# Performance work log

Measured on AMD Instinct MI355X. Metric: run time of the kernel, lower is better.

The kernel has to match this reference:

```python
import jax, jax.numpy as jnp
import numpy as np

B = 8192          # batch
CIN = 256         # in_channels
COUT = 64         # out_channels
K = 3             # kernel_size
NK = 4            # num_kernels
HIDDEN = int(CIN * 0.25)   # attention hidden = int(in_channels*ratio) = 64
TEMP = 34.0       # attention temperature
KAN_IN = 64 * 4   # base*4 = flattened conv output (COUT*2*2)
GRID_SIZE, SPLINE_ORDER = 5, 3
GMIN, GMAX = -1.0, 1.0
NUM_BASES = GRID_SIZE + SPLINE_ORDER  # 8


def setup_inputs() -> dict:
    key = jax.random.key(0)
    ks = jax.random.split(key, 8)
    s = 0.05
    return {
        "x": jax.random.normal(ks[0], (B, CIN, 4, 4), jnp.float32),
        # dynamic-conv kernel bank [num_kernels, out, in, k, k]
        "weight": jax.random.normal(ks[1], (NK, COUT, CIN, K, K), jnp.float32) * s,
        "bias": jnp.zeros((NK, COUT), jnp.float32),
        # Attention2D: GAP -> fc1 (1x1 conv == linear) -> ReLU -> fc2 -> softmax(/T)
        "fc1_w": jax.random.normal(ks[2], (HIDDEN, CIN), jnp.float32) * s,
        "fc1_b": jnp.zeros((HIDDEN,), jnp.float32),
        "fc2_w": jax.random.normal(ks[3], (NK, HIDDEN), jnp.float32) * s,
        "fc2_b": jnp.zeros((NK,), jnp.float32),
        # KANLinear params (efficient-KAN style)
        "kan_base_w": jax.random.normal(ks[4], (COUT, KAN_IN), jnp.float32) * s,
        "kan_spline_w": jax.random.normal(ks[5], (COUT, KAN_IN, NUM_BASES), jnp.float32) * s,
        "kan_spline_scaler": jnp.ones((COUT, KAN_IN), jnp.float32),
    }


def _bspline_bases(x):
    """Cox-de Boor B-spline bases; x [B, F] -> [B, F, GRID_SIZE+SPLINE_ORDER]."""
    h = (GMAX - GMIN) / GRID_SIZE
    # extended grid, shared across features: length grid_size + 2*order + 1 = 12
    grid = jnp.arange(-SPLINE_ORDER, GRID_SIZE + SPLINE_ORDER + 1, dtype=x.dtype) * h + GMIN
    xe = x[..., None]  # [B, F, 1]
    bases = ((xe >= grid[:-1]) & (xe < grid[1:])).astype(x.dtype)  # order 0
    for k in range(1, SPLINE_ORDER + 1):
        left = (xe - grid[: -(k + 1)]) / (grid[k:-1] - grid[: -(k + 1)]) * bases[..., :-1]
        right = (grid[k + 1:] - xe) / (grid[k + 1:] - grid[1:-k]) * bases[..., 1:]
        bases = left + right
    return bases  # [B, F, 8]


def reference(x, weight, bias, fc1_w, fc1_b, fc2_w, fc2_b,
              kan_base_w, kan_spline_w, kan_spline_scaler):
    b = x.shape[0]
    # --- Attention2D: softmax over kernel bank ---
    pooled = x.mean(axis=(2, 3))                                  # [B, CIN]
    hid = jax.nn.relu(pooled @ fc1_w.T + fc1_b)                   # [B, HIDDEN]
    attn = jax.nn.softmax((hid @ fc2_w.T + fc2_b) / TEMP, axis=-1)  # [B, NK]
    # --- per-sample dynamic conv, fused form ---
    # sum_k a[b,k] * conv(x, W_k) == conv with per-sample aggregated weight
    w_all = weight.reshape(NK * COUT, CIN, K, K)
    y = jax.lax.conv_general_dilated(
        x, w_all, window_strides=(1, 1), padding="VALID",
        dimension_numbers=("NCHW", "OIHW", "NCHW"))                # [B, NK*COUT, 2, 2]
    y = y.reshape(b, NK, COUT, y.shape[-2], y.shape[-1])
    conv_out = jnp.einsum("bk,bkohw->bohw", attn, y)
    conv_out = conv_out + (attn @ bias)[:, :, None, None]          # aggregated bias
    # --- KANLinear on flattened conv output ---
    feat = conv_out.reshape(b, -1)                                 # [B, 256]
    base_out = jax.nn.silu(feat) @ kan_base_w.T                    # [B, COUT]
    bases = _bspline_bases(feat)                                   # [B, 256, 8]
    spline_out = jnp.einsum("big,oig->bo", bases,
                            kan_spline_w * kan_spline_scaler[..., None])
    return base_out + spline_out                                   # [B, COUT]
```

## Files before the change

kernel.cpp:

```cpp
#include <hip/hip_runtime.h>

#define BT   8192
#define MS   16
#define XBUF (MS * 656)

typedef _Float16 half8  __attribute__((ext_vector_type(8)));
typedef _Float16 half4v __attribute__((ext_vector_type(4)));
typedef float    floatx4  __attribute__((ext_vector_type(4)));
typedef float    floatx16 __attribute__((ext_vector_type(16)));

__global__ __launch_bounds__(256) void prep_kernel(
    const float* __restrict__ weight, const float* __restrict__ base_w,
    const float* __restrict__ spline_w, const float* __restrict__ scaler,
    const float* __restrict__ fc1_w,
    _Float16* __restrict__ W3, _Float16* __restrict__ Wk3,
    _Float16* __restrict__ Wf3)
{
    const int bb = blockIdx.x;
    const int tid = threadIdx.x;
    if (bb < 256) {
        const int n = bb;
        const int c = tid;
        const float* src = weight + ((size_t)n * 256 + c) * 9;
        const int cc = c >> 5, ci = c & 31;
        #pragma unroll
        for (int ij = 0; ij < 9; ++ij) {
            W3[((size_t)(cc * 9 + ij) * 256 + n) * 32 + ci] = (_Float16)src[ij];
        }
    } else if (bb < 328) {
        const int st = bb - 256;
        #pragma unroll
        for (int u = 0; u < 8; ++u) {
            const int idx = u * 256 + tid;
            const int n = idx >> 5, kk = idx & 31;
            const int k = st * 32 + kk;
            float v;
            if (k < 256) {
                v = base_w[n * 256 + k];
            } else {
                const int r = k - 256;
                const int i = r >> 3, g = r & 7;
                v = spline_w[((size_t)n * 256 + i) * 8 + g] * scaler[n * 256 + i];
            }
            Wk3[(size_t)st * 2048 + idx] = (_Float16)v;
        }
    } else {
        const int st2 = bb - 328;
        #pragma unroll
        for (int u = 0; u < 8; ++u) {
            const int idx = u * 256 + tid;
            const int n = idx >> 5, kk = idx & 31;
            Wf3[(size_t)st2 * 2048 + idx] = (_Float16)fc1_w[n * 256 + st2 * 32 + kk];
        }
    }
}

__device__ __forceinline__ void bases8c(float xv, _Float16* dst) {
    const float t = (xv + 2.2f) * 2.5f;
    const float ft = floorf(t);
    const int idx = (int)ft;
    const float u = t - ft, v = 1.f - u;
    const float u2 = u * u, v2 = v * v;
    const float c3 = u2 * u * (1.f / 6.f);
    const float c2 = (1.f / 6.f) + 0.5f * (u + u2 - u2 * u);
    const float c1 = (1.f / 6.f) + 0.5f * (v + v2 - v2 * v);
    const float c0 = v2 * v * (1.f / 6.f);
    half8 hb;
    #pragma unroll
    for (int tt = 0; tt < 8; ++tt) {
        const int d = idx - tt;
        float b = 0.f;
        b = (d == 0) ? c3 : b;
        b = (d == 1) ? c2 : b;
        b = (d == 2) ? c1 : b;
        b = (d == 3) ? c0 : b;
        hb[tt] = (_Float16)b;
    }
    *(half8*)dst = hb;
}

__global__ __launch_bounds__(512, 4) void fused_kernel(
    const float* __restrict__ x, const _Float16* __restrict__ W3,
    const _Float16* __restrict__ Wk3, const _Float16* __restrict__ Wf3,
    const float* __restrict__ bias, const float* __restrict__ fc1_b,
    const float* __restrict__ fc2_w, const float* __restrict__ fc2_b,
    float* __restrict__ out)
{
    __shared__ __align__(16) char smem[MS * 2312 * 2];
    __shared__ float hid_lds[MS * 68];
    __shared__ float attn_s[MS][4];

    _Float16* Xs  = (_Float16*)smem;
    _Float16* Pl  = (_Float16*)(smem + 2 * XBUF * 2);
    _Float16* Act = (_Float16*)smem;

    const int tid = threadIdx.x;
    const int wv = tid >> 6, lane = tid & 63;
    const int nl = lane & 15, q = lane >> 4;
    const int cg = wv & 3, rh = wv >> 2;
    const int b0i = blockIdx.x * MS;

    const int posr = nl & 3;
    const int aLane = (nl >> 2) * 656 + ((posr >> 1) * 4 + (posr & 1)) * 40 + q * 8;
    const int lbW0 = (((rh * 2 + 0) * 4 + cg) * 16 + nl) * 32 + q * 8;
    const int lbW1 = (((rh * 2 + 1) * 4 + cg) * 16 + nl) * 32 + q * 8;

    const int s_ = tid >> 5, cch = tid & 31;
    const float* xg = x + ((size_t)(b0i + s_) * 256 + cch) * 16;

    floatx4 acc[4][2];
    #pragma unroll
    for (int rt = 0; rt < 4; ++rt) {
        acc[rt][0] = floatx4{0.f, 0.f, 0.f, 0.f};
        acc[rt][1] = floatx4{0.f, 0.f, 0.f, 0.f};
    }

    half8 bA0 = *(const half8*)(W3 + lbW0);
    half8 bB0 = *(const half8*)(W3 + lbW1);
    half8 bA1 = *(const half8*)(W3 + 8192 + lbW0);
    half8 bB1 = *(const half8*)(W3 + 8192 + lbW1);

    floatx16 r = *(const floatx16*)xg;
    {
        _Float16* xd = &Xs[s_ * 656 + cch];
        #pragma unroll
        for (int p = 0; p < 16; ++p) xd[p * 40] = (_Float16)r[p];
        float sm = 0.f;
        #pragma unroll
        for (int p = 0; p < 16; ++p) sm += r[p];
        Pl[s_ * 264 + cch] = (_Float16)(sm * (1.0f / 16.0f));
    }
    r = *(const floatx16*)(xg + 512);
    __syncthreads();

    #pragma unroll 1
    for (int cc = 0; cc < 8; ++cc) {
        const int cur = cc & 1;
        if (cc < 7) {
            _Float16* xd = &Xs[(cur ^ 1) * XBUF + s_ * 656 + cch];
            #pragma unroll
            for (int p = 0; p < 16; ++p) xd[p * 40] = (_Float16)r[p];
            float sm = 0.f;
            #pragma unroll
            for (int p = 0; p < 16; ++p) sm += r[p];
            Pl[s_ * 264 + (cc + 1) * 32 + cch] = (_Float16)(sm * (1.0f / 16.0f));
        }
        if (cc < 6) r = *(const floatx16*)(xg + (cc + 2) * 512);

        const _Float16* wst = W3 + (size_t)cc * 9 * 8192;
        const _Float16* xb = &Xs[cur * XBUF + aLane];

        const int p0tab[9] = {0, 1, 2, 4, 5, 6, 8, 9, 10};

        half8 aC0 = *(const half8*)&xb[0 * 2624];
        half8 aC1 = *(const half8*)&xb[1 * 2624];
        half8 aC2 = *(const half8*)&xb[2 * 2624];
        half8 aC3 = *(const half8*)&xb[3 * 2624];

        #pragma unroll
        for (int ij = 0; ij < 9; ++ij) {
            half8 bA2, bB2;
            {
                const _Float16* wnx = (cc * 9 + ij + 2 < 72)
                                    ? (wst + (size_t)(ij + 2) * 8192)
                                    : W3;
                bA2 = *(const half8*)(wnx + lbW0);
                bB2 = *(const half8*)(wnx + lbW1);
            }
            half8 aN0, aN1, aN2, aN3;
            if (ij < 8) {
                const int pn = p0tab[ij + 1] * 40;
                aN0 = *(const half8*)&xb[0 * 2624 + pn];
                aN1 = *(const half8*)&xb[1 * 2624 + pn];
                aN2 = *(const half8*)&xb[2 * 2624 + pn];
                aN3 = *(const half8*)&xb[3 * 2624 + pn];
            }
            acc[0][0] = __builtin_amdgcn_mfma_f32_16x16x32_f16(aC0, bA0, acc[0][0], 0, 0, 0);
            acc[0][1] = __builtin_amdgcn_mfma_f32_16x16x32_f16(aC0, bB0, acc[0][1], 0, 0, 0);
            acc[1][0] = __builtin_amdgcn_mfma_f32_16x16x32_f16(aC1, bA0, acc[1][0], 0, 0, 0);
            acc[1][1] = __builtin_amdgcn_mfma_f32_16x16x32_f16(aC1, bB0, acc[1][1], 0, 0, 0);
            acc[2][0] = __builtin_amdgcn_mfma_f32_16x16x32_f16(aC2, bA0, acc[2][0], 0, 0, 0);
            acc[2][1] = __builtin_amdgcn_mfma_f32_16x16x32_f16(aC2, bB0, acc[2][1], 0, 0, 0);
            acc[3][0] = __builtin_amdgcn_mfma_f32_16x16x32_f16(aC3, bA0, acc[3][0], 0, 0, 0);
            acc[3][1] = __builtin_amdgcn_mfma_f32_16x16x32_f16(aC3, bB0, acc[3][1], 0, 0, 0);
            bA0 = bA1; bB0 = bB1; bA1 = bA2; bB1 = bB2;
            if (ij < 8) { aC0 = aN0; aC1 = aN1; aC2 = aN2; aC3 = aN3; }
        }
        __syncthreads();
    }

    if (rh == 0) {
        floatx4 a1 = floatx4{0.f, 0.f, 0.f, 0.f};
        const _Float16* wfb = Wf3 + ((cg * 16 + nl) * 32 + q * 8);
        const _Float16* pb = &Pl[nl * 264 + q * 8];
        #pragma unroll
        for (int st = 0; st < 8; ++st) {
            const half8 aF = *(const half8*)(pb + st * 32);
            const half8 bF = *(const half8*)(wfb + st * 2048);
            a1 = __builtin_amdgcn_mfma_f32_16x16x32_f16(aF, bF, a1, 0, 0, 0);
        }
        const int h = cg * 16 + nl;
        const float fb = fc1_b[h];
        #pragma unroll
        for (int reg = 0; reg < 4; ++reg)
            hid_lds[(q * 4 + reg) * 68 + h] = fmaxf(a1[reg] + fb, 0.f);
    }
    __syncthreads();

    if (wv == 0) {
        const int s = lane >> 2, kb = lane & 3;
        float l = fc2_b[kb];
        #pragma unroll 8
        for (int h = 0; h < 64; ++h) l += hid_lds[s * 68 + h] * fc2_w[kb * 64 + h];
        float m = fmaxf(l, __shfl_xor(l, 1));
        m = fmaxf(m, __shfl_xor(m, 2));
        const float e = __expf((l - m) * (1.0f / 34.0f));
        float sm = e + __shfl_xor(e, 1);
        sm += __shfl_xor(sm, 2);
        attn_s[s][kb] = e / sm;
    }
    __syncthreads();

    const int o = cg * 16 + nl;
    if (rh == 1) {
        #pragma unroll
        for (int rt = 0; rt < 4; ++rt) {
            const int s = rt * 4 + q;
            const float a2w = attn_s[s][2], a3w = attn_s[s][3];
            #pragma unroll
            for (int e = 0; e < 4; ++e) {
                float* slot = (float*)&Act[s * 2312 + 256 + (o * 4 + e) * 8];
                slot[0] = a2w * acc[rt][0][e] + a3w * acc[rt][1][e];
            }
        }
    }
    __syncthreads();

    if (rh == 0) {
        const float bb0 = bias[o], bb1 = bias[64 + o], bb2 = bias[128 + o], bb3 = bias[192 + o];
        #pragma unroll
        for (int rt = 0; rt < 4; ++rt) {
            const int s = rt * 4 + q;
            const float a0 = attn_s[s][0], a1 = attn_s[s][1],
                        a2 = attn_s[s][2], a3 = attn_s[s][3];
            const float badd = a0 * bb0 + a1 * bb1 + a2 * bb2 + a3 * bb3;
            float f[4];
            #pragma unroll
            for (int e = 0; e < 4; ++e) {
                const float part = ((float*)&Act[s * 2312 + 256 + (o * 4 + e) * 8])[0];
                f[e] = a0 * acc[rt][0][e] + a1 * acc[rt][1][e] + part + badd;
            }
            half4v sv;
            #pragma unroll
            for (int e = 0; e < 4; ++e) {
                const float ex = __expf(-f[e]);
                sv[e] = (_Float16)(f[e] * __builtin_amdgcn_rcpf(1.f + ex));
            }
            *(half4v*)&Act[s * 2312 + o * 4] = sv;
            #pragma unroll
            for (int e = 0; e < 4; ++e)
                bases8c(f[e], &Act[s * 2312 + 256 + (o * 4 + e) * 8]);
        }
    }
    __syncthreads();

    {
        floatx4 a2 = floatx4{0.f, 0.f, 0.f, 0.f};
        const _Float16* wkb = Wk3 + ((size_t)(cg * 16 + nl) * 32 + q * 8);
        const _Float16* ab = &Act[nl * 2312 + q * 8];
        const int st0 = rh * 36;
        half8 kb0 = *(const half8*)(wkb + (size_t)st0 * 2048);
        half8 kb1 = *(const half8*)(wkb + (size_t)(st0 + 1) * 2048);
        #pragma unroll 4
        for (int i = 0; i < 36; ++i) {
            half8 kb2;
            if (i < 34) kb2 = *(const half8*)(wkb + (size_t)(st0 + i + 2) * 2048);
            const half8 aF = *(const half8*)(ab + (st0 + i) * 32);
            a2 = __builtin_amdgcn_mfma_f32_16x16x32_f16(aF, kb0, a2, 0, 0, 0);
            kb0 = kb1; kb1 = kb2;
        }
        if (rh == 1) *(floatx4*)&hid_lds[cg * 256 + lane * 4] = a2;
        __syncthreads();
        if (rh == 0) {
            const floatx4 p = *(const floatx4*)&hid_lds[cg * 256 + lane * 4];
            a2 = a2 + p;
            #pragma unroll
            for (int reg = 0; reg < 4; ++reg)
                out[(size_t)(b0i + q * 4 + reg) * 64 + cg * 16 + nl] = a2[reg];
        }
    }
}

extern "C" void kernel_launch(void* const* d_in, const int* in_sizes, int n_in,
                              void* d_out, int out_size, void* d_ws, size_t ws_size,
                              hipStream_t stream) {
    const float* x          = (const float*)d_in[0];
    const float* weight     = (const float*)d_in[1];
    const float* bias       = (const float*)d_in[2];
    const float* fc1_w      = (const float*)d_in[3];
    const float* fc1_b      = (const float*)d_in[4];
    const float* fc2_w      = (const float*)d_in[5];
    const float* fc2_b      = (const float*)d_in[6];
    const float* kan_base_w = (const float*)d_in[7];
    const float* kan_spline = (const float*)d_in[8];
    const float* kan_scaler = (const float*)d_in[9];
    float* out = (float*)d_out;

    _Float16* W3  = (_Float16*)d_ws;
    _Float16* Wk3 = W3 + (size_t)72 * 8192;
    _Float16* Wf3 = Wk3 + (size_t)72 * 2048;

    prep_kernel<<<336, 256, 0, stream>>>(weight, kan_base_w, kan_spline,
                                         kan_scaler, fc1_w, W3, Wk3, Wf3);
    fused_kernel<<<BT / MS, 512, 0, stream>>>(x, W3, Wk3, Wf3, bias, fc1_b,
                                              fc2_w, fc2_b, out);
}
```

Baseline: 246.6 us.

## Vectorize x staging with shuffle pooling and split epilogue across all waves

The x staging now uses floatx4 loads and half4 LDS stores, and the pooled means are reduced with cross-lane shuffles instead of per-thread sums over 16 scalars. The epilogue changes too: both row-halves write raw accumulator partials to LDS, and all 8 waves then compute the attention-weighted combine, SiLU and B-spline bases, each thread handling 8 features of one sample. This drops one barrier and the idle half of the waves in the epilogue. The A-operand prefetch in the MFMA loop is removed in favour of direct loads each iteration, which may expose LDS latency.

```diff
diff --git a/kernel.cpp b/kernel.cpp
--- a/kernel.cpp
+++ b/kernel.cpp
@@ -6,8 +6,8 @@
 
 typedef _Float16 half8  __attribute__((ext_vector_type(8)));
 typedef _Float16 half4v __attribute__((ext_vector_type(4)));
+typedef float    floatx2  __attribute__((ext_vector_type(2)));
 typedef float    floatx4  __attribute__((ext_vector_type(4)));
-typedef float    floatx16 __attribute__((ext_vector_type(16)));
 
 __global__ __launch_bounds__(256) void prep_kernel(
     const float* __restrict__ weight, const float* __restrict__ base_w,
@@ -105,8 +105,9 @@
     const int lbW0 = (((rh * 2 + 0) * 4 + cg) * 16 + nl) * 32 + q * 8;
     const int lbW1 = (((rh * 2 + 1) * 4 + cg) * 16 + nl) * 32 + q * 8;
 
-    const int s_ = tid >> 5, cch = tid & 31;
-    const float* xg = x + ((size_t)(b0i + s_) * 256 + cch) * 16;
+    const int s_ = tid >> 5, w32 = tid & 31;
+    const int qd = w32 & 7, pq = w32 >> 3;
+    const float* xg = x + ((size_t)(b0i + s_) * 256 + qd * 4) * 16 + pq * 4;
 
     floatx4 acc[4][2];
     #pragma unroll
@@ -120,71 +121,82 @@
     half8 bA1 = *(const half8*)(W3 + 8192 + lbW0);
     half8 bB1 = *(const half8*)(W3 + 8192 + lbW1);
 
-    floatx16 r = *(const floatx16*)xg;
-    {
-        _Float16* xd = &Xs[s_ * 656 + cch];
-        #pragma unroll
-        for (int p = 0; p < 16; ++p) xd[p * 40] = (_Float16)r[p];
-        float sm = 0.f;
-        #pragma unroll
-        for (int p = 0; p < 16; ++p) sm += r[p];
-        Pl[s_ * 264 + cch] = (_Float16)(sm * (1.0f / 16.0f));
-    }
-    r = *(const floatx16*)(xg + 512);
+    floatx4 r0, r1, r2, r3;
+    #define STAGE_POOL(bf, ch)                                             \
+    {                                                                      \
+        _Float16* xd = &Xs[(bf) * XBUF + s_ * 656 + qd * 4];               \
+        _Pragma("unroll")                                                  \
+        for (int pl = 0; pl < 4; ++pl) {                                   \
+            half4v w;                                                      \
+            w[0] = (_Float16)r0[pl]; w[1] = (_Float16)r1[pl];              \
+            w[2] = (_Float16)r2[pl]; w[3] = (_Float16)r3[pl];              \
+            *(half4v*)&xd[(pq * 4 + pl) * 40] = w;                         \
+        }                                                                  \
+        float p0s = r0[0] + r0[1] + r0[2] + r0[3];                         \
+        float p1s = r1[0] + r1[1] + r1[2] + r1[3];                         \
+        float p2s = r2[0] + r2[1] + r2[2] + r2[3];                         \
+        float p3s = r3[0] + r3[1] + r3[2] + r3[3];                         \
+        p0s += __shfl_xor(p0s, 8);  p1s += __shfl_xor(p1s, 8);             \
+        p2s += __shfl_xor(p2s, 8);  p3s += __shfl_xor(p3s, 8);             \
+        p0s += __shfl_xor(p0s, 16); p1s += __shfl_xor(p1s, 16);            \
+        p2s += __shfl_xor(p2s, 16); p3s += __shfl_xor(p3s, 16);            \
+        if (pq == 0) {                                                     \
+            half4v pw;                                                     \
+            pw[0] = (_Float16)(p0s * 0.0625f);                             \
+            pw[1] = (_Float16)(p1s * 0.0625f);                             \
+            pw[2] = (_Float16)(p2s * 0.0625f);                             \
+            pw[3] = (_Float16)(p3s * 0.0625f);                             \
+            *(half4v*)&Pl[s_ * 264 + (ch) * 32 + qd * 4] = pw;             \
+        }                                                                  \
+    }
+
+    r0 = *(const floatx4*)(xg);
+    r1 = *(const floatx4*)(xg + 16);
+    r2 = *(const floatx4*)(xg + 32);
+    r3 = *(const floatx4*)(xg + 48);
+    STAGE_POOL(0, 0)
+    r0 = *(const floatx4*)(xg + 512);
+    r1 = *(const floatx4*)(xg + 512 + 16);
+    r2 = *(const floatx4*)(xg + 512 + 32);
+    r3 = *(const floatx4*)(xg + 512 + 48);
     __syncthreads();
 
     #pragma unroll 1
     for (int cc = 0; cc < 8; ++cc) {
         const int cur = cc & 1;
-        if (cc < 7) {
-            _Float16* xd = &Xs[(cur ^ 1) * XBUF + s_ * 656 + cch];
-            #pragma unroll
-            for (int p = 0; p < 16; ++p) xd[p * 40] = (_Float16)r[p];
-            float sm = 0.f;
-            #pragma unroll
-            for (int p = 0; p < 16; ++p) sm += r[p];
-            Pl[s_ * 264 + (cc + 1) * 32 + cch] = (_Float16)(sm * (1.0f / 16.0f));
-        }
-        if (cc < 6) r = *(const floatx16*)(xg + (cc + 2) * 512);
+        if (cc < 7) STAGE_POOL(cur ^ 1, cc + 1)
+        if (cc < 6) {
+            const float* xn = xg + (cc + 2) * 512;
+            r0 = *(const floatx4*)(xn);
+            r1 = *(const floatx4*)(xn + 16);
+            r2 = *(const floatx4*)(xn + 32);
+            r3 = *(const floatx4*)(xn + 48);
+        }
 
         const _Float16* wst = W3 + (size_t)cc * 9 * 8192;
         const _Float16* xb = &Xs[cur * XBUF + aLane];
 
         const int p0tab[9] = {0, 1, 2, 4, 5, 6, 8, 9, 10};
 
-        half8 aC0 = *(const half8*)&xb[0 * 2624];
-        half8 aC1 = *(const half8*)&xb[1 * 2624];
-        half8 aC2 = *(const half8*)&xb[2 * 2624];
-        half8 aC3 = *(const half8*)&xb[3 * 2624];
-
         #pragma unroll
         for (int ij = 0; ij < 9; ++ij) {
-            half8 bA2, bB2;
-            {
-                const _Float16* wnx = (cc * 9 + ij + 2 < 72)
-                                    ? (wst + (size_t)(ij + 2) * 8192)
-                                    : W3;
-                bA2 = *(const half8*)(wnx + lbW0);
-                bB2 = *(const half8*)(wnx + lbW1);
+            const _Float16* wnx = (cc * 9 + ij + 2 < 72)
+                                ? (wst + (size_t)(ij + 2) * 8192)
+                                : W3;
+            half8 bA2 = *(const half8*)(wnx + lbW0);
+            half8 bB2 = *(const half8*)(wnx + lbW1);
+
+            const int p0 = p0tab[ij];
+            half8 aF[4];
+            #pragma unroll
+            for (int rt = 0; rt < 4; ++rt)
+                aF[rt] = *(const half8*)&xb[rt * 2624 + p0 * 40];
+            #pragma unroll
+            for (int rt = 0; rt < 4; ++rt) {
+                acc[rt][0] = __builtin_amdgcn_mfma_f32_16x16x32_f16(aF[rt], bA0, acc[rt][0], 0, 0, 0);
+                acc[rt][1] = __builtin_amdgcn_mfma_f32_16x16x32_f16(aF[rt], bB0, acc[rt][1], 0, 0, 0);
             }
-            half8 aN0, aN1, aN2, aN3;
-            if (ij < 8) {
-                const int pn = p0tab[ij + 1] * 40;
-                aN0 = *(const half8*)&xb[0 * 2624 + pn];
-                aN1 = *(const half8*)&xb[1 * 2624 + pn];
-                aN2 = *(const half8*)&xb[2 * 2624 + pn];
-                aN3 = *(const half8*)&xb[3 * 2624 + pn];
-            }
-            acc[0][0] = __builtin_amdgcn_mfma_f32_16x16x32_f16(aC0, bA0, acc[0][0], 0, 0, 0);
-            acc[0][1] = __builtin_amdgcn_mfma_f32_16x16x32_f16(aC0, bB0, acc[0][1], 0, 0, 0);
-            acc[1][0] = __builtin_amdgcn_mfma_f32_16x16x32_f16(aC1, bA0, acc[1][0], 0, 0, 0);
-            acc[1][1] = __builtin_amdgcn_mfma_f32_16x16x32_f16(aC1, bB0, acc[1][1], 0, 0, 0);
-            acc[2][0] = __builtin_amdgcn_mfma_f32_16x16x32_f16(aC2, bA0, acc[2][0], 0, 0, 0);
-            acc[2][1] = __builtin_amdgcn_mfma_f32_16x16x32_f16(aC2, bB0, acc[2][1], 0, 0, 0);
-            acc[3][0] = __builtin_amdgcn_mfma_f32_16x16x32_f16(aC3, bA0, acc[3][0], 0, 0, 0);
-            acc[3][1] = __builtin_amdgcn_mfma_f32_16x16x32_f16(aC3, bB0, acc[3][1], 0, 0, 0);
             bA0 = bA1; bB0 = bB1; bA1 = bA2; bB1 = bB2;
-            if (ij < 8) { aC0 = aN0; aC1 = aN1; aC2 = aN2; aC3 = aN3; }
         }
         __syncthreads();
     }
@@ -219,48 +231,41 @@
         sm += __shfl_xor(sm, 2);
         attn_s[s][kb] = e / sm;
     }
+    const int o = cg * 16 + nl;
+    #pragma unroll
+    for (int rt = 0; rt < 4; ++rt) {
+        const int s = rt * 4 + q;
+        #pragma unroll
+        for (int e = 0; e < 4; ++e) {
+            floatx2 pr; pr[0] = acc[rt][0][e]; pr[1] = acc[rt][1][e];
+            float* fp = (float*)&Act[s * 2312 + 256 + ((o * 4 + e) * 8)];
+            *(floatx2*)(fp + rh * 2) = pr;
+        }
+    }
     __syncthreads();
 
-    const int o = cg * 16 + nl;
-    if (rh == 1) {
-        #pragma unroll
-        for (int rt = 0; rt < 4; ++rt) {
-            const int s = rt * 4 + q;
-            const float a2w = attn_s[s][2], a3w = attn_s[s][3];
-            #pragma unroll
-            for (int e = 0; e < 4; ++e) {
-                float* slot = (float*)&Act[s * 2312 + 256 + (o * 4 + e) * 8];
-                slot[0] = a2w * acc[rt][0][e] + a3w * acc[rt][1][e];
-            }
-        }
-    }
-    __syncthreads();
-
-    if (rh == 0) {
-        const float bb0 = bias[o], bb1 = bias[64 + o], bb2 = bias[128 + o], bb3 = bias[192 + o];
-        #pragma unroll
-        for (int rt = 0; rt < 4; ++rt) {
-            const int s = rt * 4 + q;
-            const float a0 = attn_s[s][0], a1 = attn_s[s][1],
-                        a2 = attn_s[s][2], a3 = attn_s[s][3];
-            const float badd = a0 * bb0 + a1 * bb1 + a2 * bb2 + a3 * bb3;
-            float f[4];
-            #pragma unroll
-            for (int e = 0; e < 4; ++e) {
-                const float part = ((float*)&Act[s * 2312 + 256 + (o * 4 + e) * 8])[0];
-                f[e] = a0 * acc[rt][0][e] + a1 * acc[rt][1][e] + part + badd;
-            }
-            half4v sv;
-            #pragma unroll
-            for (int e = 0; e < 4; ++e) {
-                const float ex = __expf(-f[e]);
-                sv[e] = (_Float16)(f[e] * __builtin_amdgcn_rcpf(1.f + ex));
-            }
-            *(half4v*)&Act[s * 2312 + o * 4] = sv;
-            #pragma unroll
-            for (int e = 0; e < 4; ++e)
-                bases8c(f[e], &Act[s * 2312 + 256 + (o * 4 + e) * 8]);
-        }
+    {
+        const int sl = lane >> 5, fl = lane & 31;
+        const int s = wv * 2 + sl;
+        const float a0 = attn_s[s][0], a1 = attn_s[s][1],
+                    a2 = attn_s[s][2], a3 = attn_s[s][3];
+        const int o0 = fl * 2, f0 = fl * 8;
+        const float badd0 = a0 * bias[o0] + a1 * bias[64 + o0]
+                          + a2 * bias[128 + o0] + a3 * bias[192 + o0];
+        const float badd1 = a0 * bias[o0 + 1] + a1 * bias[64 + o0 + 1]
+                          + a2 * bias[128 + o0 + 1] + a3 * bias[192 + o0 + 1];
+        half8 sv;
+        #pragma unroll
+        for (int u = 0; u < 8; ++u) {
+            float* fp = (float*)&Act[s * 2312 + 256 + (f0 + u) * 8];
+            const floatx4 P = *(const floatx4*)fp;
+            const float fv = a0 * P[0] + a1 * P[1] + a2 * P[2] + a3 * P[3]
+                           + ((u < 4) ? badd0 : badd1);
+            const float ex = __expf(-fv);
+            sv[u] = (_Float16)(fv * __builtin_amdgcn_rcpf(1.f + ex));
+            bases8c(fv, (_Float16*)fp);
+        }
+        *(half8*)&Act[s * 2312 + o0 * 4] = sv;
     }
     __syncthreads();
 
```

New measurement: 247.8 us. Within noise of the previous version (+0.5%).
